# Kernel optimization log

Measured on AMD Instinct MI355X. Metric: run time of the kernel, lower is better.

The kernel has to match this reference:

```python
import jax, jax.numpy as jnp
import numpy as np

L2_REG = 0.25

def setup_inputs() -> dict:
    key = jax.random.key(0)
    k0, k1, k2, k3 = jax.random.split(key, 4)
    B, D, A, K = 16384, 128, 8192, 64
    image_embed = jax.random.normal(k0, (B, D), dtype=jnp.float32)
    anc_ind = jax.random.randint(k1, (A,), 0, B, dtype=jnp.int64)
    pos_ind = jax.random.randint(k2, (A,), 0, B, dtype=jnp.int64)
    neg_ind = jax.random.randint(k3, (A, K), 0, B, dtype=jnp.int64)
    return {"image_embed": image_embed, "anc_ind": anc_ind,
            "pos_ind": pos_ind, "neg_ind": neg_ind}

def reference(image_embed, anc_ind, pos_ind, neg_ind):
    # Gather anchor/positive/negative embeddings
    a = image_embed[anc_ind]          # [A, D]
    p = image_embed[pos_ind]          # [A, D]
    n = image_embed[neg_ind]          # [A, K, D]
    # inner[i, k] = a_i . (n_ik - p_i)
    inner = jnp.einsum('ad,akd->ak', a, n - p[:, None, :])  # [A, K]
    # log(1 + sum_k exp(inner)) computed stably via logaddexp(0, logsumexp)
    per_anchor = jnp.logaddexp(jnp.float32(0.0), jax.nn.logsumexp(inner, axis=1))
    npair = jnp.mean(per_anchor)
    # l2 term: mean L2 norm of all batch embeddings, added once per anchor / len -> once
    l2 = L2_REG * jnp.mean(jnp.linalg.norm(image_embed, axis=1))
    return npair + l2
```

## Files before the change

kernel.cpp:

```cpp
#include <hip/hip_runtime.h>
#include <math.h>

#define B_SZ 16384
#define D_DIM 128
#define A_SZ 8192
#define K_SZ 64
#define L2_REG_F 0.25f
#define CONV_BLK 2048
#define NBLK 2048

typedef float vfloat2 __attribute__((ext_vector_type(2)));

__device__ __forceinline__ float wave_reduce_sum(float v) {
    #pragma unroll
    for (int off = 32; off > 0; off >>= 1)
        v += __shfl_xor(v, off, 64);
    return v;
}

__device__ __forceinline__ float wave_reduce_max(float v) {
    #pragma unroll
    for (int off = 32; off > 0; off >>= 1)
        v = fmaxf(v, __shfl_xor(v, off, 64));
    return v;
}

__device__ __forceinline__ void dequant16(uint4 q, float4& o0, float4& o1,
                                          float4& o2, float4& o3) {
    vfloat2 f0 = __builtin_amdgcn_cvt_pk_f32_fp8(q.x, false);
    vfloat2 f1 = __builtin_amdgcn_cvt_pk_f32_fp8(q.x, true);
    vfloat2 f2 = __builtin_amdgcn_cvt_pk_f32_fp8(q.y, false);
    vfloat2 f3 = __builtin_amdgcn_cvt_pk_f32_fp8(q.y, true);
    vfloat2 f4 = __builtin_amdgcn_cvt_pk_f32_fp8(q.z, false);
    vfloat2 f5 = __builtin_amdgcn_cvt_pk_f32_fp8(q.z, true);
    vfloat2 f6 = __builtin_amdgcn_cvt_pk_f32_fp8(q.w, false);
    vfloat2 f7 = __builtin_amdgcn_cvt_pk_f32_fp8(q.w, true);
    o0 = make_float4(f0.x, f0.y, f1.x, f1.y);
    o1 = make_float4(f2.x, f2.y, f3.x, f3.y);
    o2 = make_float4(f4.x, f4.y, f5.x, f5.y);
    o3 = make_float4(f6.x, f6.y, f7.x, f7.y);
}

__device__ __forceinline__ float dot4(float4 a, float4 b) {
    return a.x * b.x + a.y * b.y + a.z * b.z + a.w * b.w;
}

__global__ __launch_bounds__(256) void convert_kernel(const float* __restrict__ embed,
                                                      unsigned short* __restrict__ tab,
                                                      float* __restrict__ partial) {
    __shared__ float red[4];
    const int wave = threadIdx.x >> 6;
    const int lane = threadIdx.x & 63;
    const int gw   = blockIdx.x * 4 + wave;
    float acc = 0.f;
    #pragma unroll
    for (int r = 0; r < 2; ++r) {
        const int row = gw * 2 + r;
        const float2* rr = (const float2*)(embed + (size_t)row * D_DIM);
        float2 v = rr[lane];
        acc += sqrtf(wave_reduce_sum(v.x * v.x + v.y * v.y));
        unsigned pk = (unsigned)__builtin_amdgcn_cvt_pk_fp8_f32(v.x, v.y, 0, false);
        tab[(size_t)row * 64 + lane] = (unsigned short)pk;
    }
    if (lane == 0) red[wave] = acc * (L2_REG_F / (float)B_SZ);
    __syncthreads();
    if (threadIdx.x == 0)
        partial[blockIdx.x] = red[0] + red[1] + red[2] + red[3];
}

__global__ __launch_bounds__(256) void npair_kernel(const unsigned short* __restrict__ tab,
                                                    const int* __restrict__ anc_ind,
                                                    const int* __restrict__ pos_ind,
                                                    const int* __restrict__ neg_ind,
                                                    float* __restrict__ partial) {
    __shared__ float red[4];
    const int wave = threadIdx.x >> 6;
    const int lane = threadIdx.x & 63;
    const int i    = blockIdx.x * 4 + wave;
    const int g = lane >> 3;
    const int c = lane & 7;

    const int ai = anc_ind[i];
    const int pi = pos_ind[i];
    const int nid_all = neg_ind[(size_t)i * K_SZ + lane];

    uint4 ua4 = ((const uint4*)(tab + (size_t)ai * 64))[c];
    uint4 up4 = ((const uint4*)(tab + (size_t)pi * 64))[c];

    int nidx[8];
    #pragma unroll
    for (int p = 0; p < 8; ++p)
        nidx[p] = __shfl(nid_all, p * 8 + g, 64);

    uint4 q[8];
    #pragma unroll
    for (int p = 0; p < 8; ++p)
        q[p] = ((const uint4*)(tab + (size_t)nidx[p] * 64))[c];

    float4 A0, A1, A2, A3;
    dequant16(ua4, A0, A1, A2, A3);

    float4 P0, P1, P2, P3;
    dequant16(up4, P0, P1, P2, P3);
    float ap = dot4(A0, P0) + dot4(A1, P1) + dot4(A2, P2) + dot4(A3, P3);
    ap += __shfl_xor(ap, 1, 64);
    ap += __shfl_xor(ap, 2, 64);
    ap += __shfl_xor(ap, 4, 64);

    float inner = 0.f;
    #pragma unroll
    for (int p = 0; p < 8; ++p) {
        float4 N0, N1, N2, N3;
        dequant16(q[p], N0, N1, N2, N3);
        float s = dot4(A0, N0) + dot4(A1, N1) + dot4(A2, N2) + dot4(A3, N3);
        s += __shfl_xor(s, 1, 64);
        s += __shfl_xor(s, 2, 64);
        s += __shfl_xor(s, 4, 64);
        if (c == p) inner = s;
    }
    inner -= ap;

    float m  = wave_reduce_max(inner);
    float se = wave_reduce_sum(__expf(inner - m));
    float lse = m + __logf(se);
    float per = (lse > 0.f) ? lse + log1pf(__expf(-lse)) : log1pf(__expf(lse));

    if (lane == 0) red[wave] = per * (1.0f / (float)A_SZ);
    __syncthreads();
    if (threadIdx.x == 0)
        partial[blockIdx.x] = red[0] + red[1] + red[2] + red[3];
}

__global__ __launch_bounds__(256) void f32_kernel(const float* __restrict__ embed,
                                                  const int* __restrict__ anc_ind,
                                                  const int* __restrict__ pos_ind,
                                                  const int* __restrict__ neg_ind,
                                                  float* __restrict__ partial) {
    __shared__ __align__(16) float a_lds[4][D_DIM];
    __shared__ float red[4];
    const int wave = threadIdx.x >> 6;
    const int lane = threadIdx.x & 63;
    const int gw   = blockIdx.x * 4 + wave;

    float acc_l2 = 0.f;
    #pragma unroll
    for (int r = 0; r < 2; ++r) {
        const int row = gw * 2 + r;
        const float2* rr = (const float2*)(embed + (size_t)row * D_DIM);
        float2 v = rr[lane];
        acc_l2 += sqrtf(wave_reduce_sum(v.x * v.x + v.y * v.y));
    }
    const int i  = gw;
    const int ai = anc_ind[i];
    const int pi = pos_ind[i];
    const int ni = neg_ind[(size_t)i * K_SZ + lane];
    const float2* ar = (const float2*)(embed + (size_t)ai * D_DIM);
    const float2* pr = (const float2*)(embed + (size_t)pi * D_DIM);
    float2 a2 = ar[lane];
    float2 p2 = pr[lane];
    a_lds[wave][2 * lane]     = a2.x;
    a_lds[wave][2 * lane + 1] = a2.y;
    float ap = wave_reduce_sum(a2.x * p2.x + a2.y * p2.y);
    const float4* nr = (const float4*)(embed + (size_t)ni * D_DIM);
    const float4* al = (const float4*)a_lds[wave];
    float s0 = 0.f, s1 = 0.f, s2 = 0.f, s3 = 0.f;
    #pragma unroll
    for (int j = 0; j < D_DIM / 4; j += 4) {
        float4 n0 = nr[j], n1 = nr[j + 1], n2 = nr[j + 2], n3 = nr[j + 3];
        float4 a0 = al[j], a1 = al[j + 1], a2v = al[j + 2], a3 = al[j + 3];
        s0 += dot4(a0, n0); s1 += dot4(a1, n1);
        s2 += dot4(a2v, n2); s3 += dot4(a3, n3);
    }
    float inner = (s0 + s1) + (s2 + s3) - ap;
    float m  = wave_reduce_max(inner);
    float se = wave_reduce_sum(__expf(inner - m));
    float lse = m + __logf(se);
    float per = (lse > 0.f) ? lse + log1pf(__expf(-lse)) : log1pf(__expf(lse));
    float combined = per * (1.0f / (float)A_SZ) + acc_l2 * (L2_REG_F / (float)B_SZ);
    if (lane == 0) red[wave] = combined;
    __syncthreads();
    if (threadIdx.x == 0)
        partial[blockIdx.x] = red[0] + red[1] + red[2] + red[3];
}

__global__ __launch_bounds__(256) void finalize_kernel(const float* __restrict__ partial,
                                                       int n, float* __restrict__ out) {
    __shared__ float red[4];
    const int wave = threadIdx.x >> 6;
    const int lane = threadIdx.x & 63;
    float v = 0.f;
    for (int j = threadIdx.x; j < n; j += 256) v += partial[j];
    v = wave_reduce_sum(v);
    if (lane == 0) red[wave] = v;
    __syncthreads();
    if (threadIdx.x == 0)
        out[0] = red[0] + red[1] + red[2] + red[3];
}

extern "C" void kernel_launch(void* const* d_in, const int* in_sizes, int n_in,
                              void* d_out, int out_size, void* d_ws, size_t ws_size,
                              hipStream_t stream) {
    const float* embed = (const float*)d_in[0];
    const int*   anc   = (const int*)d_in[1];
    const int*   pos   = (const int*)d_in[2];
    const int*   neg   = (const int*)d_in[3];
    float* out = (float*)d_out;

    const size_t tab_bytes = (size_t)B_SZ * D_DIM;
    const size_t need = tab_bytes + (CONV_BLK + NBLK) * sizeof(float);

    if (ws_size >= need) {
        unsigned short* tab = (unsigned short*)d_ws;
        float* partial = (float*)((char*)d_ws + tab_bytes);
        convert_kernel<<<CONV_BLK, 256, 0, stream>>>(embed, tab, partial);
        npair_kernel<<<NBLK, 256, 0, stream>>>(tab, anc, pos, neg, partial + CONV_BLK);
        finalize_kernel<<<1, 256, 0, stream>>>(partial, CONV_BLK + NBLK, out);
    } else {
        float* partial = (float*)d_ws;
        f32_kernel<<<NBLK, 256, 0, stream>>>(embed, anc, pos, neg, partial);
        finalize_kernel<<<1, 256, 0, stream>>>(partial, NBLK, out);
    }
}
```

Baseline: 81.31 us.

## Fuse convert, npair and finalize into one kernel with grid barrier

Merges the fp8 conversion, the npair loss and the final reduction into a single persistent-style kernel of 1024 blocks. A hierarchical atomic grid barrier separates table conversion from the gather phase, and a last-block-done counter performs the final sum. Each wave now handles four rows and two anchors. This removes two kernel launches and their inter-kernel gaps, but adds a memset, a spin-wait barrier that depends on all 1024 blocks being co-resident, and a timeout break that could silently read a partially written table.

```diff
diff --git a/kernel.cpp b/kernel.cpp
--- a/kernel.cpp
+++ b/kernel.cpp
@@ -6,8 +6,10 @@
 #define A_SZ 8192
 #define K_SZ 64
 #define L2_REG_F 0.25f
-#define CONV_BLK 2048
-#define NBLK 2048
+#define GRID_BLKS 1024
+#define GROUPS 32
+#define BLKS_PER_GROUP 32
+#define CNT_STRIDE 32
 
 typedef float vfloat2 __attribute__((ext_vector_type(2)));
 
@@ -45,90 +47,137 @@
     return a.x * b.x + a.y * b.y + a.z * b.z + a.w * b.w;
 }
 
-__global__ __launch_bounds__(256) void convert_kernel(const float* __restrict__ embed,
-                                                      unsigned short* __restrict__ tab,
-                                                      float* __restrict__ partial) {
+__global__ __launch_bounds__(256, 4) void fused_kernel(
+    const float* __restrict__ embed,
+    const int* __restrict__ anc_ind,
+    const int* __restrict__ pos_ind,
+    const int* __restrict__ neg_ind,
+    unsigned char* __restrict__ tab,
+    float* __restrict__ partial,
+    unsigned* __restrict__ cnt,
+    float* __restrict__ out) {
     __shared__ float red[4];
+    __shared__ int is_final;
     const int wave = threadIdx.x >> 6;
     const int lane = threadIdx.x & 63;
-    const int gw   = blockIdx.x * 4 + wave;
-    float acc = 0.f;
-    #pragma unroll
-    for (int r = 0; r < 2; ++r) {
-        const int row = gw * 2 + r;
-        const float2* rr = (const float2*)(embed + (size_t)row * D_DIM);
-        float2 v = rr[lane];
-        acc += sqrtf(wave_reduce_sum(v.x * v.x + v.y * v.y));
-        unsigned pk = (unsigned)__builtin_amdgcn_cvt_pk_fp8_f32(v.x, v.y, 0, false);
-        tab[(size_t)row * 64 + lane] = (unsigned short)pk;
-    }
-    if (lane == 0) red[wave] = acc * (L2_REG_F / (float)B_SZ);
-    __syncthreads();
-    if (threadIdx.x == 0)
-        partial[blockIdx.x] = red[0] + red[1] + red[2] + red[3];
-}
-
-__global__ __launch_bounds__(256) void npair_kernel(const unsigned short* __restrict__ tab,
-                                                    const int* __restrict__ anc_ind,
-                                                    const int* __restrict__ pos_ind,
-                                                    const int* __restrict__ neg_ind,
-                                                    float* __restrict__ partial) {
-    __shared__ float red[4];
-    const int wave = threadIdx.x >> 6;
-    const int lane = threadIdx.x & 63;
-    const int i    = blockIdx.x * 4 + wave;
+    const int blk  = blockIdx.x;
+    const int w    = blk * 4 + wave;
+
+    float acc_l2 = 0.f;
+    {
+        const int sub = lane >> 4;
+        const int j   = lane & 15;
+        const int row = w * 4 + sub;
+        const float4* rp = (const float4*)(embed + (size_t)row * D_DIM + j * 8);
+        float4 va = rp[0], vb = rp[1];
+        float ss = dot4(va, va) + dot4(vb, vb);
+        ss += __shfl_xor(ss, 1, 64);
+        ss += __shfl_xor(ss, 2, 64);
+        ss += __shfl_xor(ss, 4, 64);
+        ss += __shfl_xor(ss, 8, 64);
+        if (j == 0) acc_l2 = sqrtf(ss);
+        unsigned u0 = __builtin_amdgcn_cvt_pk_fp8_f32(va.x, va.y, 0, false);
+        u0 = __builtin_amdgcn_cvt_pk_fp8_f32(va.z, va.w, u0, true);
+        unsigned u1 = __builtin_amdgcn_cvt_pk_fp8_f32(vb.x, vb.y, 0, false);
+        u1 = __builtin_amdgcn_cvt_pk_fp8_f32(vb.z, vb.w, u1, true);
+        ((uint2*)(tab + (size_t)row * D_DIM))[j] = make_uint2(u0, u1);
+    }
+
+    __syncthreads();
+    if (threadIdx.x == 0) {
+        __threadfence();
+        unsigned* gc   = cnt + (blk >> 5) * CNT_STRIDE;
+        unsigned* root = cnt + GROUPS * CNT_STRIDE;
+        if (atomicAdd(gc, 1u) == BLKS_PER_GROUP - 1)
+            atomicAdd(root, 1u);
+        long t = 0;
+        while (__hip_atomic_load(root, __ATOMIC_RELAXED,
+                                 __HIP_MEMORY_SCOPE_AGENT) < GROUPS) {
+            __builtin_amdgcn_s_sleep(8);
+            if (++t > (1L << 24)) break;
+        }
+        __threadfence();
+    }
+    __syncthreads();
+
     const int g = lane >> 3;
     const int c = lane & 7;
-
-    const int ai = anc_ind[i];
-    const int pi = pos_ind[i];
-    const int nid_all = neg_ind[(size_t)i * K_SZ + lane];
-
-    uint4 ua4 = ((const uint4*)(tab + (size_t)ai * 64))[c];
-    uint4 up4 = ((const uint4*)(tab + (size_t)pi * 64))[c];
-
-    int nidx[8];
-    #pragma unroll
-    for (int p = 0; p < 8; ++p)
-        nidx[p] = __shfl(nid_all, p * 8 + g, 64);
-
-    uint4 q[8];
-    #pragma unroll
-    for (int p = 0; p < 8; ++p)
-        q[p] = ((const uint4*)(tab + (size_t)nidx[p] * 64))[c];
-
-    float4 A0, A1, A2, A3;
-    dequant16(ua4, A0, A1, A2, A3);
-
-    float4 P0, P1, P2, P3;
-    dequant16(up4, P0, P1, P2, P3);
-    float ap = dot4(A0, P0) + dot4(A1, P1) + dot4(A2, P2) + dot4(A3, P3);
-    ap += __shfl_xor(ap, 1, 64);
-    ap += __shfl_xor(ap, 2, 64);
-    ap += __shfl_xor(ap, 4, 64);
-
-    float inner = 0.f;
-    #pragma unroll
-    for (int p = 0; p < 8; ++p) {
-        float4 N0, N1, N2, N3;
-        dequant16(q[p], N0, N1, N2, N3);
-        float s = dot4(A0, N0) + dot4(A1, N1) + dot4(A2, N2) + dot4(A3, N3);
-        s += __shfl_xor(s, 1, 64);
-        s += __shfl_xor(s, 2, 64);
-        s += __shfl_xor(s, 4, 64);
-        if (c == p) inner = s;
-    }
-    inner -= ap;
-
-    float m  = wave_reduce_max(inner);
-    float se = wave_reduce_sum(__expf(inner - m));
-    float lse = m + __logf(se);
-    float per = (lse > 0.f) ? lse + log1pf(__expf(-lse)) : log1pf(__expf(lse));
-
-    if (lane == 0) red[wave] = per * (1.0f / (float)A_SZ);
-    __syncthreads();
-    if (threadIdx.x == 0)
-        partial[blockIdx.x] = red[0] + red[1] + red[2] + red[3];
+    float acc_np = 0.f;
+    #pragma unroll
+    for (int t = 0; t < 2; ++t) {
+        const int i  = w * 2 + t;
+        const int ai = anc_ind[i];
+        const int pi = pos_ind[i];
+        const int nid_all = neg_ind[(size_t)i * K_SZ + lane];
+
+        uint4 ua4 = ((const uint4*)(tab + (size_t)ai * D_DIM))[c];
+        uint4 up4 = ((const uint4*)(tab + (size_t)pi * D_DIM))[c];
+
+        int nidx[8];
+        #pragma unroll
+        for (int p = 0; p < 8; ++p)
+            nidx[p] = __shfl(nid_all, p * 8 + g, 64);
+
+        uint4 q[8];
+        #pragma unroll
+        for (int p = 0; p < 8; ++p)
+            q[p] = ((const uint4*)(tab + (size_t)nidx[p] * D_DIM))[c];
+
+        float4 A0, A1, A2, A3;
+        dequant16(ua4, A0, A1, A2, A3);
+        float4 P0, P1, P2, P3;
+        dequant16(up4, P0, P1, P2, P3);
+        float ap = dot4(A0, P0) + dot4(A1, P1) + dot4(A2, P2) + dot4(A3, P3);
+        ap += __shfl_xor(ap, 1, 64);
+        ap += __shfl_xor(ap, 2, 64);
+        ap += __shfl_xor(ap, 4, 64);
+
+        float inner = 0.f;
+        #pragma unroll
+        for (int p = 0; p < 8; ++p) {
+            float4 N0, N1, N2, N3;
+            dequant16(q[p], N0, N1, N2, N3);
+            float s = dot4(A0, N0) + dot4(A1, N1) + dot4(A2, N2) + dot4(A3, N3);
+            s += __shfl_xor(s, 1, 64);
+            s += __shfl_xor(s, 2, 64);
+            s += __shfl_xor(s, 4, 64);
+            if (c == p) inner = s;
+        }
+        inner -= ap;
+
+        float m  = wave_reduce_max(inner);
+        float se = wave_reduce_sum(__expf(inner - m));
+        float lse = m + __logf(se);
+        acc_np += (lse > 0.f) ? lse + log1pf(__expf(-lse)) : log1pf(__expf(lse));
+    }
+
+    float contrib = acc_l2 * (L2_REG_F / (float)B_SZ)
+                  + ((lane == 0) ? acc_np * (1.0f / (float)A_SZ) : 0.f);
+    contrib = wave_reduce_sum(contrib);
+    if (lane == 0) red[wave] = contrib;
+    if (threadIdx.x == 0) is_final = 0;
+    __syncthreads();
+    if (threadIdx.x == 0) {
+        partial[blk] = red[0] + red[1] + red[2] + red[3];
+        __threadfence();
+        unsigned* gc2   = cnt + (GROUPS + 1 + (blk >> 5)) * CNT_STRIDE;
+        unsigned* root2 = cnt + (2 * GROUPS + 1) * CNT_STRIDE;
+        if (atomicAdd(gc2, 1u) == BLKS_PER_GROUP - 1)
+            if (atomicAdd(root2, 1u) == GROUPS - 1)
+                is_final = 1;
+    }
+    __syncthreads();
+    if (is_final) {
+        if (threadIdx.x == 0) __threadfence();
+        __syncthreads();
+        float v = partial[threadIdx.x]       + partial[threadIdx.x + 256]
+                + partial[threadIdx.x + 512] + partial[threadIdx.x + 768];
+        v = wave_reduce_sum(v);
+        if (lane == 0) red[wave] = v;
+        __syncthreads();
+        if (threadIdx.x == 0)
+            out[0] = red[0] + red[1] + red[2] + red[3];
+    }
 }
 
 __global__ __launch_bounds__(256) void f32_kernel(const float* __restrict__ embed,
@@ -206,18 +255,21 @@
     const int*   neg   = (const int*)d_in[3];
     float* out = (float*)d_out;
 
-    const size_t tab_bytes = (size_t)B_SZ * D_DIM;
-    const size_t need = tab_bytes + (CONV_BLK + NBLK) * sizeof(float);
+    const size_t tab_bytes  = (size_t)B_SZ * D_DIM;
+    const size_t part_bytes = GRID_BLKS * sizeof(float);
+    const size_t cnt_bytes  = (size_t)(2 * GROUPS + 2) * CNT_STRIDE * sizeof(unsigned);
+    const size_t need = tab_bytes + part_bytes + cnt_bytes;
 
     if (ws_size >= need) {
-        unsigned short* tab = (unsigned short*)d_ws;
-        float* partial = (float*)((char*)d_ws + tab_bytes);
-        convert_kernel<<<CONV_BLK, 256, 0, stream>>>(embed, tab, partial);
-        npair_kernel<<<NBLK, 256, 0, stream>>>(tab, anc, pos, neg, partial + CONV_BLK);
-        finalize_kernel<<<1, 256, 0, stream>>>(partial, CONV_BLK + NBLK, out);
+        unsigned char* tab = (unsigned char*)d_ws;
+        float* partial = (float*)(tab + tab_bytes);
+        unsigned* cnt  = (unsigned*)((char*)partial + part_bytes);
+        hipMemsetAsync(cnt, 0, cnt_bytes, stream);
+        fused_kernel<<<GRID_BLKS, 256, 0, stream>>>(embed, anc, pos, neg,
+                                                    tab, partial, cnt, out);
     } else {
         float* partial = (float*)d_ws;
-        f32_kernel<<<NBLK, 256, 0, stream>>>(embed, anc, pos, neg, partial);
-        finalize_kernel<<<1, 256, 0, stream>>>(partial, NBLK, out);
-    }
-}
+        f32_kernel<<<2048, 256, 0, stream>>>(embed, anc, pos, neg, partial);
+        finalize_kernel<<<1, 256, 0, stream>>>(partial, 2048, out);
+    }
+}
```

Result: slower. 141.3 us (+73.7%).
